# Performance work log

Hardware: AMD Instinct MI355X
Metric: run time of the kernel (lower is better)

Reference implementation:

```python
import jax, jax.numpy as jnp
import numpy as np

N_NODES = 100000


def sage_conv(x, src, dst, w_self, w_nei, b):
    # mean aggregation over incoming edges (src -> dst)
    agg = jax.ops.segment_sum(x[src], dst, num_segments=N_NODES)          # [N, d]
    deg = jax.ops.segment_sum(jnp.ones((src.shape[0], 1), x.dtype), dst,
                              num_segments=N_NODES)                        # [N, 1]
    mean = agg / jnp.maximum(deg, 1.0)
    return x @ w_self + mean @ w_nei + b


def setup_inputs() -> dict:
    key = jax.random.key(0)
    ks = jax.random.split(key, 12)
    d_in, d_hid, d_out = 64, 64, 64
    E = 1600000
    s = lambda d: 1.0 / np.sqrt(d)
    return {
        "x": jax.random.normal(ks[0], (N_NODES, d_in), jnp.float32),
        "edge_index": jax.random.randint(ks[1], (2, E), 0, N_NODES, jnp.int64),
        "w_self1": jax.random.normal(ks[2], (d_in, d_hid), jnp.float32) * s(d_in),
        "w_nei1": jax.random.normal(ks[3], (d_in, d_hid), jnp.float32) * s(d_in),
        "b1": jnp.zeros((d_hid,), jnp.float32),
        "w_self2": jax.random.normal(ks[4], (d_hid, d_hid), jnp.float32) * s(d_hid),
        "w_nei2": jax.random.normal(ks[5], (d_hid, d_hid), jnp.float32) * s(d_hid),
        "b2": jnp.zeros((d_hid,), jnp.float32),
        "w_self3": jax.random.normal(ks[6], (d_hid, d_out), jnp.float32) * s(d_hid),
        "w_nei3": jax.random.normal(ks[7], (d_hid, d_out), jnp.float32) * s(d_hid),
        "b3": jnp.zeros((d_out,), jnp.float32),
    }


def reference(x, edge_index, w_self1, w_nei1, b1, w_self2, w_nei2, b2,
              w_self3, w_nei3, b3):
    src, dst = edge_index[0], edge_index[1]
    h = jax.nn.relu(sage_conv(x, src, dst, w_self1, w_nei1, b1))
    h = jax.nn.relu(sage_conv(h, src, dst, w_self2, w_nei2, b2))
    h = sage_conv(h, src, dst, w_self3, w_nei3, b3)
    return h
```

## Files before the change

### kernel.cpp

```cpp
#include <hip/hip_runtime.h>
#include <hip/hip_bf16.h>

#define PB   512
#define CAP  5120

typedef short bf16x8 __attribute__((ext_vector_type(8)));
typedef float f32x4  __attribute__((ext_vector_type(4)));

__device__ __forceinline__ unsigned short f2bf(float f) {
    unsigned u = __float_as_uint(f);
    u += 0x7FFFu + ((u >> 16) & 1u);
    return (unsigned short)(u >> 16);
}

__global__ __launch_bounds__(256) void bucket_scatter(const int* __restrict__ src,
                                                      const int* __restrict__ dst,
                                                      int* __restrict__ gcount,
                                                      int* __restrict__ pairs,
                                                      int E, int NB) {
    __shared__ int h[512];
    const int tid = threadIdx.x;
    for (int i = tid; i < NB; i += 256) h[i] = 0;
    __syncthreads();
    const int per = (E + PB - 1) / PB;
    const int s = blockIdx.x * per;
    const int e = min(E, s + per);
    for (int i = s + tid; i < e; i += 256) atomicAdd(&h[dst[i] >> 8], 1);
    __syncthreads();
    for (int b = tid; b < NB; b += 256) {
        const int c = h[b];
        h[b] = (c > 0) ? atomicAdd(&gcount[b], c) : 0;
    }
    __syncthreads();
    for (int i = s + tid; i < e; i += 256) {
        const int d = dst[i];
        const int b = d >> 8;
        const int slot = atomicAdd(&h[b], 1);
        if (slot < CAP)
            pairs[(size_t)b * CAP + slot] = src[i] | ((d & 255) << 20);
    }
}

__global__ __launch_bounds__(256) void csr_finalize(const int* __restrict__ pairs,
                                                    const int* __restrict__ gcount,
                                                    int2* __restrict__ rowrange,
                                                    int* __restrict__ col, int N) {
    __shared__ int sp[CAP];
    __shared__ int h[256];
    __shared__ int tmp[256];
    __shared__ int cur[256];
    const int tid = threadIdx.x;
    const int b = blockIdx.x;
    const size_t base = (size_t)b * CAP;
    const int cnt = min(gcount[b], (int)CAP);

    for (int i = tid; i < cnt; i += 256) sp[i] = pairs[base + i];
    h[tid] = 0;
    __syncthreads();
    for (int i = tid; i < cnt; i += 256)
        atomicAdd(&h[(sp[i] >> 20) & 255], 1);
    __syncthreads();
    const int v = h[tid];
    tmp[tid] = v;
    __syncthreads();
    for (int off = 1; off < 256; off <<= 1) {
        int t = (tid >= off) ? tmp[tid - off] : 0;
        __syncthreads();
        tmp[tid] += t;
        __syncthreads();
    }
    const int excl = tmp[tid] - v;
    const int node = (b << 8) + tid;
    if (node < N) rowrange[node] = make_int2((int)base + excl, (int)base + excl + v);
    cur[tid] = excl;
    __syncthreads();
    for (int i = tid; i < cnt; i += 256) {
        const int p = sp[i];
        const int slot = atomicAdd(&cur[(p >> 20) & 255], 1);
        col[base + slot] = p & 0xFFFFF;
    }
}

__global__ __launch_bounds__(256) void prep_kernel(
        const float* __restrict__ x, unsigned short* __restrict__ xb, int n8,
        const float* __restrict__ Ws1, const float* __restrict__ Wn1,
        const float* __restrict__ Ws2, const float* __restrict__ Wn2,
        const float* __restrict__ Ws3, const float* __restrict__ Wn3,
        unsigned short* __restrict__ bw) {
    if (blockIdx.x < 96) {
        const int i = blockIdx.x * 256 + threadIdx.x;
        const int w = i >> 13;
        const int r = i & 8191;
        const float* Ws = (w == 0) ? Ws1 : (w == 1) ? Ws2 : Ws3;
        const float* Wn = (w == 0) ? Wn1 : (w == 1) ? Wn2 : Wn3;
        const int j = r & 7;
        const int L = (r >> 3) & 63;
        const int t = (r >> 9) & 3;
        const int s = r >> 11;
        const int k = s * 32 + ((L >> 4) << 3) + j;
        const int n = t * 16 + (L & 15);
        const float v = (k < 64) ? Ws[k * 64 + n] : Wn[(k - 64) * 64 + n];
        bw[i] = f2bf(v);
    } else {
        const int g = (blockIdx.x - 96) * 256 + threadIdx.x;
        if (g >= n8) return;
        const float4 v0 = *(const float4*)(x + (size_t)g * 8);
        const float4 v1 = *(const float4*)(x + (size_t)g * 8 + 4);
        uint4 o;
        o.x = (unsigned)f2bf(v0.x) | ((unsigned)f2bf(v0.y) << 16);
        o.y = (unsigned)f2bf(v0.z) | ((unsigned)f2bf(v0.w) << 16);
        o.z = (unsigned)f2bf(v1.x) | ((unsigned)f2bf(v1.y) << 16);
        o.w = (unsigned)f2bf(v1.z) | ((unsigned)f2bf(v1.w) << 16);
        *(uint4*)(xb + (size_t)g * 8) = o;
    }
}

#define ACC8U(A, V)                                                   \
    A[0] += __uint_as_float((V).x << 16);                             \
    A[1] += __uint_as_float((V).x & 0xFFFF0000u);                     \
    A[2] += __uint_as_float((V).y << 16);                             \
    A[3] += __uint_as_float((V).y & 0xFFFF0000u);                     \
    A[4] += __uint_as_float((V).z << 16);                             \
    A[5] += __uint_as_float((V).z & 0xFFFF0000u);                     \
    A[6] += __uint_as_float((V).w << 16);                             \
    A[7] += __uint_as_float((V).w & 0xFFFF0000u);

__global__ __launch_bounds__(128) void sage_fused_kernel(
        const unsigned short* __restrict__ xin, const int* __restrict__ col,
        const int2* __restrict__ rowrange,
        const unsigned short* __restrict__ bswp, const float* __restrict__ bias,
        unsigned short* __restrict__ outb,
        float* __restrict__ outf,
        int N, int do_relu) {
    __shared__ __align__(16) unsigned short smean[32][72];

    const int tid = threadIdx.x;
    const int node0 = blockIdx.x * 32;
    const int lane = tid & 63;

    {
        const int nl = tid >> 2;
        const int node = node0 + nl;
        const int c16 = (tid & 3) * 16;
        float accA[8] = {0.f}, accB[8] = {0.f};
        float accC[8] = {0.f}, accD[8] = {0.f};
        float rd = 0.f;
        if (node < N) {
            const int2 rr = rowrange[node];
            const int beg = rr.x;
            const int end = rr.y;
            int i = beg;
            for (; i + 4 <= end; i += 4) {
                const int s0 = col[i + 0];
                const int s1 = col[i + 1];
                const int s2 = col[i + 2];
                const int s3 = col[i + 3];
                const unsigned short* p0 = xin + (size_t)s0 * 64 + c16;
                const unsigned short* p1 = xin + (size_t)s1 * 64 + c16;
                const unsigned short* p2 = xin + (size_t)s2 * 64 + c16;
                const unsigned short* p3 = xin + (size_t)s3 * 64 + c16;
                const uint4 a0 = *(const uint4*)(p0);
                const uint4 b0 = *(const uint4*)(p0 + 8);
                const uint4 a1 = *(const uint4*)(p1);
                const uint4 b1 = *(const uint4*)(p1 + 8);
                const uint4 a2 = *(const uint4*)(p2);
                const uint4 b2 = *(const uint4*)(p2 + 8);
                const uint4 a3 = *(const uint4*)(p3);
                const uint4 b3 = *(const uint4*)(p3 + 8);
                ACC8U(accA, a0) ACC8U(accB, b0)
                ACC8U(accC, a1) ACC8U(accD, b1)
                ACC8U(accA, a2) ACC8U(accB, b2)
                ACC8U(accC, a3) ACC8U(accD, b3)
            }
            for (; i < end; ++i) {
                const unsigned short* p = xin + (size_t)col[i] * 64 + c16;
                const uint4 a = *(const uint4*)(p);
                const uint4 b = *(const uint4*)(p + 8);
                ACC8U(accA, a) ACC8U(accB, b)
            }
            rd = 1.0f / fmaxf((float)(end - beg), 1.0f);
        }
        uint4 o0, o1;
        {
            float m[8];
#pragma unroll
            for (int k = 0; k < 8; ++k) m[k] = (accA[k] + accC[k]) * rd;
            o0.x = (unsigned)f2bf(m[0]) | ((unsigned)f2bf(m[1]) << 16);
            o0.y = (unsigned)f2bf(m[2]) | ((unsigned)f2bf(m[3]) << 16);
            o0.z = (unsigned)f2bf(m[4]) | ((unsigned)f2bf(m[5]) << 16);
            o0.w = (unsigned)f2bf(m[6]) | ((unsigned)f2bf(m[7]) << 16);
#pragma unroll
            for (int k = 0; k < 8; ++k) m[k] = (accB[k] + accD[k]) * rd;
            o1.x = (unsigned)f2bf(m[0]) | ((unsigned)f2bf(m[1]) << 16);
            o1.y = (unsigned)f2bf(m[2]) | ((unsigned)f2bf(m[3]) << 16);
            o1.z = (unsigned)f2bf(m[4]) | ((unsigned)f2bf(m[5]) << 16);
            o1.w = (unsigned)f2bf(m[6]) | ((unsigned)f2bf(m[7]) << 16);
        }
        *(uint4*)(&smean[nl][c16])     = o0;
        *(uint4*)(&smean[nl][c16 + 8]) = o1;
    }
    __syncthreads();

    const int wave = tid >> 6;
    const int m    = lane & 15;
    const int quad = lane >> 4;
    const int nw0  = node0 + wave * 16;

    int arow = nw0 + m;
    if (arow >= N) arow = N - 1;
    const unsigned short* xr = xin + (size_t)arow * 64 + quad * 8;

    f32x4 acc[4];
#pragma unroll
    for (int t = 0; t < 4; ++t) {
        const float b = bias[t * 16 + m];
        acc[t] = (f32x4){b, b, b, b};
    }

#pragma unroll
    for (int s = 0; s < 4; ++s) {
        bf16x8 a;
        if (s < 2) a = *(const bf16x8*)(xr + s * 32);
        else       a = *(const bf16x8*)(&smean[wave * 16 + m][(s - 2) * 32 + quad * 8]);
#pragma unroll
        for (int t = 0; t < 4; ++t) {
            const bf16x8 bf = *(const bf16x8*)(bswp + (((s * 4 + t) * 64 + lane) << 3));
            acc[t] = __builtin_amdgcn_mfma_f32_16x16x32_bf16(a, bf, acc[t], 0, 0, 0);
        }
    }

#pragma unroll
    for (int t = 0; t < 4; ++t) {
        const int colg = t * 16 + m;
#pragma unroll
        for (int r = 0; r < 4; ++r) {
            const int node = nw0 + quad * 4 + r;
            if (node < N) {
                float v = acc[t][r];
                if (do_relu) v = fmaxf(v, 0.f);
                if (outf) outf[(size_t)node * 64 + colg] = v;
                if (outb) outb[(size_t)node * 64 + colg] = f2bf(v);
            }
        }
    }
}

extern "C" void kernel_launch(void* const* d_in, const int* in_sizes, int n_in,
                              void* d_out, int out_size, void* d_ws, size_t ws_size,
                              hipStream_t stream) {
    const float* x   = (const float*)d_in[0];
    const int*   ei  = (const int*)d_in[1];
    const float* ws1 = (const float*)d_in[2];
    const float* wn1 = (const float*)d_in[3];
    const float* b1  = (const float*)d_in[4];
    const float* ws2 = (const float*)d_in[5];
    const float* wn2 = (const float*)d_in[6];
    const float* b2  = (const float*)d_in[7];
    const float* ws3 = (const float*)d_in[8];
    const float* wn3 = (const float*)d_in[9];
    const float* b3  = (const float*)d_in[10];

    const int N = in_sizes[0] / 64;
    const int E = in_sizes[1] / 2;
    const int* src = ei;
    const int* dst = ei + E;
    const int NB = (N + 255) >> 8;

    float* out = (float*)d_out;

    auto align256 = [](size_t v) { return (v + 255) / 256 * 256; };
    char* p = (char*)d_ws;
    int*  gcount   = (int*)p;  p += align256((size_t)NB * 4);
    int*  pairs    = (int*)p;  p += align256((size_t)NB * CAP * 4);
    int*  col      = (int*)p;  p += align256((size_t)NB * CAP * 4);
    int2* rowrange = (int2*)p; p += align256((size_t)N * 8);
    unsigned short* xb  = (unsigned short*)p; p += align256((size_t)N * 64 * 2);
    unsigned short* xb2 = (unsigned short*)p; p += align256((size_t)N * 64 * 2);
    unsigned short* bw  = (unsigned short*)p; p += align256(3 * 8192 * 2);

    const int n8 = N * 64 / 8;
    const int prep_blocks = 96 + (n8 + 255) / 256;
    const int fused_blocks = (N + 31) / 32;

    hipMemsetAsync(gcount, 0, (size_t)NB * 4, stream);
    bucket_scatter<<<PB, 256, 0, stream>>>(src, dst, gcount, pairs, E, NB);
    csr_finalize  <<<NB, 256, 0, stream>>>(pairs, gcount, rowrange, col, N);

    prep_kernel<<<prep_blocks, 256, 0, stream>>>(x, xb, n8, ws1, wn1, ws2, wn2, ws3, wn3, bw);

    sage_fused_kernel<<<fused_blocks, 128, 0, stream>>>(xb,  col, rowrange, bw,         b1, xb2,     nullptr, N, 1);
    sage_fused_kernel<<<fused_blocks, 128, 0, stream>>>(xb2, col, rowrange, bw + 8192,  b2, xb,      nullptr, N, 1);
    sage_fused_kernel<<<fused_blocks, 128, 0, stream>>>(xb,  col, rowrange, bw + 16384, b3, nullptr, out,     N, 0);
}
```

Measured before the change: 256.4 us.

## Merge bucket scatter with prep, widen CSR finalize, interleave gather column split

Folds the edge bucket-scatter and the x/weight bf16 conversion into one launch, so the independent prep blocks run alongside the scatter and one kernel launch is dropped. csr_finalize now uses 512 threads per bucket to load and place edges with more parallelism, with the scan still limited to 256 threads. The gather changes each thread's 16-column slice into two 8-column chunks 32 apart, so the four threads of a node read adjacent 16-byte pieces together. This may improve how the loads coalesce. In exchange the merged kernel mixes block types with different resource needs.

After: 256.8 us. About the same (+0.2%).

```diff
diff --git a/kernel.cpp b/kernel.cpp
--- a/kernel.cpp
+++ b/kernel.cpp
@@ -13,82 +13,38 @@
     return (unsigned short)(u >> 16);
 }
 
-__global__ __launch_bounds__(256) void bucket_scatter(const int* __restrict__ src,
-                                                      const int* __restrict__ dst,
-                                                      int* __restrict__ gcount,
-                                                      int* __restrict__ pairs,
-                                                      int E, int NB) {
-    __shared__ int h[512];
-    const int tid = threadIdx.x;
-    for (int i = tid; i < NB; i += 256) h[i] = 0;
-    __syncthreads();
-    const int per = (E + PB - 1) / PB;
-    const int s = blockIdx.x * per;
-    const int e = min(E, s + per);
-    for (int i = s + tid; i < e; i += 256) atomicAdd(&h[dst[i] >> 8], 1);
-    __syncthreads();
-    for (int b = tid; b < NB; b += 256) {
-        const int c = h[b];
-        h[b] = (c > 0) ? atomicAdd(&gcount[b], c) : 0;
-    }
-    __syncthreads();
-    for (int i = s + tid; i < e; i += 256) {
-        const int d = dst[i];
-        const int b = d >> 8;
-        const int slot = atomicAdd(&h[b], 1);
-        if (slot < CAP)
-            pairs[(size_t)b * CAP + slot] = src[i] | ((d & 255) << 20);
-    }
-}
-
-__global__ __launch_bounds__(256) void csr_finalize(const int* __restrict__ pairs,
-                                                    const int* __restrict__ gcount,
-                                                    int2* __restrict__ rowrange,
-                                                    int* __restrict__ col, int N) {
-    __shared__ int sp[CAP];
-    __shared__ int h[256];
-    __shared__ int tmp[256];
-    __shared__ int cur[256];
-    const int tid = threadIdx.x;
-    const int b = blockIdx.x;
-    const size_t base = (size_t)b * CAP;
-    const int cnt = min(gcount[b], (int)CAP);
-
-    for (int i = tid; i < cnt; i += 256) sp[i] = pairs[base + i];
-    h[tid] = 0;
-    __syncthreads();
-    for (int i = tid; i < cnt; i += 256)
-        atomicAdd(&h[(sp[i] >> 20) & 255], 1);
-    __syncthreads();
-    const int v = h[tid];
-    tmp[tid] = v;
-    __syncthreads();
-    for (int off = 1; off < 256; off <<= 1) {
-        int t = (tid >= off) ? tmp[tid - off] : 0;
-        __syncthreads();
-        tmp[tid] += t;
-        __syncthreads();
-    }
-    const int excl = tmp[tid] - v;
-    const int node = (b << 8) + tid;
-    if (node < N) rowrange[node] = make_int2((int)base + excl, (int)base + excl + v);
-    cur[tid] = excl;
-    __syncthreads();
-    for (int i = tid; i < cnt; i += 256) {
-        const int p = sp[i];
-        const int slot = atomicAdd(&cur[(p >> 20) & 255], 1);
-        col[base + slot] = p & 0xFFFFF;
-    }
-}
-
-__global__ __launch_bounds__(256) void prep_kernel(
+__global__ __launch_bounds__(256) void build_and_prep(
+        const int* __restrict__ src, const int* __restrict__ dst,
+        int* __restrict__ gcount, int* __restrict__ pairs, int E, int NB,
         const float* __restrict__ x, unsigned short* __restrict__ xb, int n8,
         const float* __restrict__ Ws1, const float* __restrict__ Wn1,
         const float* __restrict__ Ws2, const float* __restrict__ Wn2,
         const float* __restrict__ Ws3, const float* __restrict__ Wn3,
         unsigned short* __restrict__ bw) {
-    if (blockIdx.x < 96) {
-        const int i = blockIdx.x * 256 + threadIdx.x;
+    const int tid = threadIdx.x;
+    if (blockIdx.x < PB) {
+        __shared__ int h[512];
+        for (int i = tid; i < NB; i += 256) h[i] = 0;
+        __syncthreads();
+        const int per = (E + PB - 1) / PB;
+        const int s = blockIdx.x * per;
+        const int e = min(E, s + per);
+        for (int i = s + tid; i < e; i += 256) atomicAdd(&h[dst[i] >> 8], 1);
+        __syncthreads();
+        for (int b = tid; b < NB; b += 256) {
+            const int c = h[b];
+            h[b] = (c > 0) ? atomicAdd(&gcount[b], c) : 0;
+        }
+        __syncthreads();
+        for (int i = s + tid; i < e; i += 256) {
+            const int d = dst[i];
+            const int b = d >> 8;
+            const int slot = atomicAdd(&h[b], 1);
+            if (slot < CAP)
+                pairs[(size_t)b * CAP + slot] = src[i] | ((d & 255) << 20);
+        }
+    } else if (blockIdx.x < PB + 96) {
+        const int i = (blockIdx.x - PB) * 256 + tid;
         const int w = i >> 13;
         const int r = i & 8191;
         const float* Ws = (w == 0) ? Ws1 : (w == 1) ? Ws2 : Ws3;
@@ -102,7 +58,7 @@
         const float v = (k < 64) ? Ws[k * 64 + n] : Wn[(k - 64) * 64 + n];
         bw[i] = f2bf(v);
     } else {
-        const int g = (blockIdx.x - 96) * 256 + threadIdx.x;
+        const int g = (blockIdx.x - PB - 96) * 256 + tid;
         if (g >= n8) return;
         const float4 v0 = *(const float4*)(x + (size_t)g * 8);
         const float4 v1 = *(const float4*)(x + (size_t)g * 8 + 4);
@@ -115,6 +71,48 @@
     }
 }
 
+__global__ __launch_bounds__(512) void csr_finalize(const int* __restrict__ pairs,
+                                                    const int* __restrict__ gcount,
+                                                    int2* __restrict__ rowrange,
+                                                    int* __restrict__ col, int N) {
+    __shared__ int sp[CAP];
+    __shared__ int h[256];
+    __shared__ int tmp[256];
+    __shared__ int cur[256];
+    const int tid = threadIdx.x;
+    const int b = blockIdx.x;
+    const size_t base = (size_t)b * CAP;
+    const int cnt = min(gcount[b], (int)CAP);
+
+    for (int i = tid; i < cnt; i += 512) sp[i] = pairs[base + i];
+    if (tid < 256) h[tid] = 0;
+    __syncthreads();
+    for (int i = tid; i < cnt; i += 512)
+        atomicAdd(&h[(sp[i] >> 20) & 255], 1);
+    __syncthreads();
+    if (tid < 256) tmp[tid] = h[tid];
+    __syncthreads();
+    for (int off = 1; off < 256; off <<= 1) {
+        int t = (tid >= off && tid < 256) ? tmp[tid - off] : 0;
+        __syncthreads();
+        if (tid < 256) tmp[tid] += t;
+        __syncthreads();
+    }
+    if (tid < 256) {
+        const int v = h[tid];
+        const int excl = tmp[tid] - v;
+        const int node = (b << 8) + tid;
+        if (node < N) rowrange[node] = make_int2((int)base + excl, (int)base + excl + v);
+        cur[tid] = excl;
+    }
+    __syncthreads();
+    for (int i = tid; i < cnt; i += 512) {
+        const int p = sp[i];
+        const int slot = atomicAdd(&cur[(p >> 20) & 255], 1);
+        col[base + slot] = p & 0xFFFFF;
+    }
+}
+
 #define ACC8U(A, V)                                                   \
     A[0] += __uint_as_float((V).x << 16);                             \
     A[1] += __uint_as_float((V).x & 0xFFFF0000u);                     \
@@ -141,7 +139,7 @@
     {
         const int nl = tid >> 2;
         const int node = node0 + nl;
-        const int c16 = (tid & 3) * 16;
+        const int o = (tid & 3) * 8;
         float accA[8] = {0.f}, accB[8] = {0.f};
         float accC[8] = {0.f}, accD[8] = {0.f};
         float rd = 0.f;
@@ -155,27 +153,27 @@
                 const int s1 = col[i + 1];
                 const int s2 = col[i + 2];
                 const int s3 = col[i + 3];
-                const unsigned short* p0 = xin + (size_t)s0 * 64 + c16;
-                const unsigned short* p1 = xin + (size_t)s1 * 64 + c16;
-                const unsigned short* p2 = xin + (size_t)s2 * 64 + c16;
-                const unsigned short* p3 = xin + (size_t)s3 * 64 + c16;
+                const unsigned short* p0 = xin + (size_t)s0 * 64 + o;
+                const unsigned short* p1 = xin + (size_t)s1 * 64 + o;
+                const unsigned short* p2 = xin + (size_t)s2 * 64 + o;
+                const unsigned short* p3 = xin + (size_t)s3 * 64 + o;
                 const uint4 a0 = *(const uint4*)(p0);
-                const uint4 b0 = *(const uint4*)(p0 + 8);
+                const uint4 b0 = *(const uint4*)(p0 + 32);
                 const uint4 a1 = *(const uint4*)(p1);
-                const uint4 b1 = *(const uint4*)(p1 + 8);
+                const uint4 b1 = *(const uint4*)(p1 + 32);
                 const uint4 a2 = *(const uint4*)(p2);
-                const uint4 b2 = *(const uint4*)(p2 + 8);
+                const uint4 b2 = *(const uint4*)(p2 + 32);
                 const uint4 a3 = *(const uint4*)(p3);
-                const uint4 b3 = *(const uint4*)(p3 + 8);
+                const uint4 b3 = *(const uint4*)(p3 + 32);
                 ACC8U(accA, a0) ACC8U(accB, b0)
                 ACC8U(accC, a1) ACC8U(accD, b1)
                 ACC8U(accA, a2) ACC8U(accB, b2)
                 ACC8U(accC, a3) ACC8U(accD, b3)
             }
             for (; i < end; ++i) {
-                const unsigned short* p = xin + (size_t)col[i] * 64 + c16;
+                const unsigned short* p = xin + (size_t)col[i] * 64 + o;
                 const uint4 a = *(const uint4*)(p);
-                const uint4 b = *(const uint4*)(p + 8);
+                const uint4 b = *(const uint4*)(p + 32);
                 ACC8U(accA, a) ACC8U(accB, b)
             }
             rd = 1.0f / fmaxf((float)(end - beg), 1.0f);
@@ -196,8 +194,8 @@
             o1.z = (unsigned)f2bf(m[4]) | ((unsigned)f2bf(m[5]) << 16);
             o1.w = (unsigned)f2bf(m[6]) | ((unsigned)f2bf(m[7]) << 16);
         }
-        *(uint4*)(&smean[nl][c16])     = o0;
-        *(uint4*)(&smean[nl][c16 + 8]) = o1;
+        *(uint4*)(&smean[nl][o])      = o0;
+        *(uint4*)(&smean[nl][o + 32]) = o1;
     }
     __syncthreads();
 
@@ -279,14 +277,14 @@
     unsigned short* bw  = (unsigned short*)p; p += align256(3 * 8192 * 2);
 
     const int n8 = N * 64 / 8;
-    const int prep_blocks = 96 + (n8 + 255) / 256;
+    const int merged_blocks = PB + 96 + (n8 + 255) / 256;
     const int fused_blocks = (N + 31) / 32;
 
     hipMemsetAsync(gcount, 0, (size_t)NB * 4, stream);
-    bucket_scatter<<<PB, 256, 0, stream>>>(src, dst, gcount, pairs, E, NB);
-    csr_finalize  <<<NB, 256, 0, stream>>>(pairs, gcount, rowrange, col, N);
-
-    prep_kernel<<<prep_blocks, 256, 0, stream>>>(x, xb, n8, ws1, wn1, ws2, wn2, ws3, wn3, bw);
+    build_and_prep<<<merged_blocks, 256, 0, stream>>>(src, dst, gcount, pairs, E, NB,
+                                                      x, xb, n8,
+                                                      ws1, wn1, ws2, wn2, ws3, wn3, bw);
+    csr_finalize<<<NB, 512, 0, stream>>>(pairs, gcount, rowrange, col, N);
 
     sage_fused_kernel<<<fused_blocks, 128, 0, stream>>>(xb,  col, rowrange, bw,         b1, xb2,     nullptr, N, 1);
     sage_fused_kernel<<<fused_blocks, 128, 0, stream>>>(xb2, col, rowrange, bw + 8192,  b2, xb,      nullptr, N, 1);
```
